# Optimization experiments

Hardware: AMD Instinct MI355X
Metric: run time of the kernel (lower is better)

## Reference

```python
import jax, jax.numpy as jnp
import numpy as np

B1, B2, CHUNK, HID, T = 64, 16, 128, 64, 131072
N_CHUNKS = 128


def setup_inputs() -> dict:
    key = jax.random.key(0)
    ks = jax.random.split(key, 12)
    # positive prices so log(p) is finite
    p = jax.random.uniform(ks[0], (T, 2), jnp.float32) * 2.0 + 0.5
    inds = jax.random.randint(ks[1], (B1,), 0, 100000, dtype=jnp.int32)
    open_slices = jax.random.randint(ks[2], (B1, B2, 1), 0, T, dtype=jnp.int32)
    ls_probs = jax.random.uniform(ks[3], (B1, B2, 1, 1), jnp.float32)
    open_probs = jax.random.uniform(ks[4], (B1, B2, 1, 1), jnp.float32)
    open_hx = jax.random.normal(ks[5], (B1, B2, 2, HID), jnp.float32) * 0.1
    s = 1.0 / np.sqrt(HID)
    # torch nn.LSTM params: gate order i,f,g,o
    W_ih = jax.random.uniform(ks[6], (4 * HID, 2), jnp.float32, -s, s)
    W_hh = jax.random.uniform(ks[7], (4 * HID, HID), jnp.float32, -s, s)
    b_ih = jax.random.uniform(ks[8], (4 * HID,), jnp.float32, -s, s)
    b_hh = jax.random.uniform(ks[9], (4 * HID,), jnp.float32, -s, s)
    W_out = jax.random.uniform(ks[10], (1, HID), jnp.float32, -s, s)
    b_out = jax.random.uniform(ks[11], (1,), jnp.float32, -s, s)
    return {"inds": inds, "p": p, "ls_probs": ls_probs, "open_probs": open_probs,
            "open_slices": open_slices, "open_hx": open_hx,
            "W_ih": W_ih, "W_hh": W_hh, "b_ih": b_ih, "b_hh": b_hh,
            "W_out": W_out, "b_out": b_out, "n_chunks": N_CHUNKS}


def reference(inds, p, ls_probs, open_probs, open_slices, open_hx,
              W_ih, W_hh, b_ih, b_hh, W_out, b_out, n_chunks):
    b1, b2 = open_hx.shape[:2]
    hid = open_hx.shape[-1]
    C = CHUNK
    h0 = open_hx[:, :, 0, :].reshape(b1 * b2, hid)
    c0 = open_hx[:, :, 1, :].reshape(b1 * b2, hid)
    open_logp = jnp.log(p[open_slices])  # (b1, b2, 1, 2)
    # sliding-window gather base: idx[i,j,t] = inds[i] + j + t (per-chunk offset added in scan)
    base = (inds[:, None, None]
            + jnp.arange(b2, dtype=inds.dtype)[None, :, None]
            + jnp.arange(C, dtype=inds.dtype)[None, None, :])  # (b1, b2, C)
    bias = b_ih + b_hh

    def lstm_chunk(x, h, c):  # x: (N, C, 2)
        xg = x @ W_ih.T + bias  # precompute input projection: (N, C, 4H)
        def step(carry, xg_t):
            h, c = carry
            g = xg_t + h @ W_hh.T
            i, f, gg, o = jnp.split(g, 4, axis=-1)
            c = jax.nn.sigmoid(f) * c + jax.nn.sigmoid(i) * jnp.tanh(gg)
            h = jax.nn.sigmoid(o) * jnp.tanh(c)
            return (h, c), h
        (h, c), hs = jax.lax.scan(step, (h, c), xg.swapaxes(0, 1))
        return hs.swapaxes(0, 1), h, c  # (N, C, H)

    def chunk_step(carry, offset):
        h, c, last_nd, loss = carry
        idx = base + offset * C                      # (b1, b2, C)
        p_chunk = p[idx]                             # (b1, b2, C, 2)
        x = p_chunk - p_chunk[:, :, :1, :]           # re-center on first step of chunk
        out, h, c = lstm_chunk(x.reshape(b1 * b2, C, 2), h, c)
        probs = jax.nn.sigmoid(out.reshape(b1, b2, C, hid) @ W_out.T + b_out)  # (b1,b2,C,1)
        not_done = last_nd * jnp.cumprod(1.0 - probs[:, :, :-1], axis=2)       # (b1,b2,C-1,1)
        probs = jnp.concatenate([probs[:, :, :1], probs[:, :, 1:] * not_done], axis=2)
        last_nd = not_done[:, :, -1:, :]
        logp = jnp.log(p_chunk)
        payoff = ls_probs * (logp - open_logp) + (1.0 - ls_probs) * (open_logp - logp)
        loss = loss + jnp.sum(open_probs * probs * payoff)
        return (h, c, last_nd, loss), None

    init = (h0, c0, jnp.ones((b1, b2, 1, 1), p.dtype), jnp.zeros((), p.dtype))
    (_, _, _, loss), _ = jax.lax.scan(chunk_step, init, jnp.arange(n_chunks))
    return loss
```

## Files before the change

kernel.cpp:

```cpp
#include <hip/hip_runtime.h>


#define CH  128
#define HID 64

__device__ __forceinline__ float rlf(float v, int l) {
  return __builtin_bit_cast(float, __builtin_amdgcn_readlane(__builtin_bit_cast(int, v), l));
}
__device__ __forceinline__ int rli(int v, int l) { return __builtin_amdgcn_readlane(v, l); }
__device__ __forceinline__ int packh(float a, float b) {
  return __builtin_bit_cast(int, __builtin_amdgcn_cvt_pkrtz(a, b));
}
__device__ __forceinline__ float frcp(float x) { return __builtin_amdgcn_rcpf(x); }
__device__ __forceinline__ float sigm(float x) { return frcp(1.0f + __expf(-x)); }
__device__ __forceinline__ float tanh_(float x) {
  float e = __expf(2.0f * x);
  return 1.0f - 2.0f * frcp(e + 1.0f);
}
template <int CTRL, int RMASK>
__device__ __forceinline__ float dpp_add(float v) {
  int x = __builtin_amdgcn_update_dpp(0, __builtin_bit_cast(int, v), CTRL, RMASK, 0xF, true);
  return v + __builtin_bit_cast(float, x);
}
__device__ __forceinline__ float dpp_xor1(float v) {
  int x = __builtin_amdgcn_update_dpp(0, __builtin_bit_cast(int, v), 0xB1, 0xF, 0xF, true);
  return __builtin_bit_cast(float, x);
}
__device__ __forceinline__ float dpp_wave_sum(float v) {
  v = dpp_add<0x111, 0xF>(v);
  v = dpp_add<0x112, 0xF>(v);
  v = dpp_add<0x114, 0xF>(v);
  v = dpp_add<0x118, 0xF>(v);
  v = dpp_add<0x142, 0xA>(v);
  v = dpp_add<0x143, 0xC>(v);
  return v;
}

#define DOTS(A, B, W) asm( \
  "v_dot2_f32_f16 %[a], %[h0], %[w0], %[a]\n\t"   \
  "v_dot2_f32_f16 %[b], %[h16], %[w16], %[b]\n\t" \
  "v_dot2_f32_f16 %[a], %[h1], %[w1], %[a]\n\t"   \
  "v_dot2_f32_f16 %[b], %[h17], %[w17], %[b]\n\t" \
  "v_dot2_f32_f16 %[a], %[h2], %[w2], %[a]\n\t"   \
  "v_dot2_f32_f16 %[b], %[h18], %[w18], %[b]\n\t" \
  "v_dot2_f32_f16 %[a], %[h3], %[w3], %[a]\n\t"   \
  "v_dot2_f32_f16 %[b], %[h19], %[w19], %[b]\n\t" \
  "v_dot2_f32_f16 %[a], %[h4], %[w4], %[a]\n\t"   \
  "v_dot2_f32_f16 %[b], %[h20], %[w20], %[b]\n\t" \
  "v_dot2_f32_f16 %[a], %[h5], %[w5], %[a]\n\t"   \
  "v_dot2_f32_f16 %[b], %[h21], %[w21], %[b]\n\t" \
  "v_dot2_f32_f16 %[a], %[h6], %[w6], %[a]\n\t"   \
  "v_dot2_f32_f16 %[b], %[h22], %[w22], %[b]\n\t" \
  "v_dot2_f32_f16 %[a], %[h7], %[w7], %[a]\n\t"   \
  "v_dot2_f32_f16 %[b], %[h23], %[w23], %[b]\n\t" \
  "v_dot2_f32_f16 %[a], %[h8], %[w8], %[a]\n\t"   \
  "v_dot2_f32_f16 %[b], %[h24], %[w24], %[b]\n\t" \
  "v_dot2_f32_f16 %[a], %[h9], %[w9], %[a]\n\t"   \
  "v_dot2_f32_f16 %[b], %[h25], %[w25], %[b]\n\t" \
  "v_dot2_f32_f16 %[a], %[h10], %[w10], %[a]\n\t" \
  "v_dot2_f32_f16 %[b], %[h26], %[w26], %[b]\n\t" \
  "v_dot2_f32_f16 %[a], %[h11], %[w11], %[a]\n\t" \
  "v_dot2_f32_f16 %[b], %[h27], %[w27], %[b]\n\t" \
  "v_dot2_f32_f16 %[a], %[h12], %[w12], %[a]\n\t" \
  "v_dot2_f32_f16 %[b], %[h28], %[w28], %[b]\n\t" \
  "v_dot2_f32_f16 %[a], %[h13], %[w13], %[a]\n\t" \
  "v_dot2_f32_f16 %[b], %[h29], %[w29], %[b]\n\t" \
  "v_dot2_f32_f16 %[a], %[h14], %[w14], %[a]\n\t" \
  "v_dot2_f32_f16 %[b], %[h30], %[w30], %[b]\n\t" \
  "v_dot2_f32_f16 %[a], %[h15], %[w15], %[a]\n\t" \
  "v_dot2_f32_f16 %[b], %[h31], %[w31], %[b]"     \
  : [a] "+v"(A), [b] "+v"(B) \
  : [h0] "s"(hs[0]),   [h1] "s"(hs[1]),   [h2] "s"(hs[2]),   [h3] "s"(hs[3]),   \
    [h4] "s"(hs[4]),   [h5] "s"(hs[5]),   [h6] "s"(hs[6]),   [h7] "s"(hs[7]),   \
    [h8] "s"(hs[8]),   [h9] "s"(hs[9]),   [h10] "s"(hs[10]), [h11] "s"(hs[11]), \
    [h12] "s"(hs[12]), [h13] "s"(hs[13]), [h14] "s"(hs[14]), [h15] "s"(hs[15]), \
    [h16] "s"(hs[16]), [h17] "s"(hs[17]), [h18] "s"(hs[18]), [h19] "s"(hs[19]), \
    [h20] "s"(hs[20]), [h21] "s"(hs[21]), [h22] "s"(hs[22]), [h23] "s"(hs[23]), \
    [h24] "s"(hs[24]), [h25] "s"(hs[25]), [h26] "s"(hs[26]), [h27] "s"(hs[27]), \
    [h28] "s"(hs[28]), [h29] "s"(hs[29]), [h30] "s"(hs[30]), [h31] "s"(hs[31]), \
    [w0] "v"(W[0]),   [w1] "v"(W[1]),   [w2] "v"(W[2]),   [w3] "v"(W[3]),   \
    [w4] "v"(W[4]),   [w5] "v"(W[5]),   [w6] "v"(W[6]),   [w7] "v"(W[7]),   \
    [w8] "v"(W[8]),   [w9] "v"(W[9]),   [w10] "v"(W[10]), [w11] "v"(W[11]), \
    [w12] "v"(W[12]), [w13] "v"(W[13]), [w14] "v"(W[14]), [w15] "v"(W[15]), \
    [w16] "v"(W[16]), [w17] "v"(W[17]), [w18] "v"(W[18]), [w19] "v"(W[19]), \
    [w20] "v"(W[20]), [w21] "v"(W[21]), [w22] "v"(W[22]), [w23] "v"(W[23]), \
    [w24] "v"(W[24]), [w25] "v"(W[25]), [w26] "v"(W[26]), [w27] "v"(W[27]), \
    [w28] "v"(W[28]), [w29] "v"(W[29]), [w30] "v"(W[30]), [w31] "v"(W[31]))

__global__ __attribute__((amdgpu_flat_work_group_size(128, 128), amdgpu_waves_per_eu(2, 2)))
void pc_lstm_kernel(const int* __restrict__ inds,
                    const float* __restrict__ p,
                    const float* __restrict__ ls_probs,
                    const float* __restrict__ open_probs,
                    const int* __restrict__ open_slices,
                    const float* __restrict__ open_hx,
                    const float* __restrict__ W_ih,
                    const float* __restrict__ W_hh,
                    const float* __restrict__ b_ih,
                    const float* __restrict__ b_hh,
                    const float* __restrict__ W_out,
                    const float* __restrict__ b_out,
                    const int* __restrict__ n_chunks_p,
                    float* __restrict__ out)
{
  __shared__ __fp16 ring[2][CH][HID];
  __shared__ int prod;
  __shared__ int cons;

  const int tid  = threadIdx.x;
  const int wv   = tid >> 6;
  const int lane = tid & 63;
  const int s    = blockIdx.x;
  const int n_chunks = n_chunks_p[0];
  const int tbase = inds[s >> 4] + (s & 15);
  const float2* p2 = (const float2*)p;

  if (tid == 0) { prod = 0; cons = 0; }
  __syncthreads();

  if (wv == 0) {
    int W0[32], W1[32], W2[32], W3[32];
    {
      const float2* r0 = (const float2*)(W_hh + (0 * HID + lane) * HID);
      const float2* r1 = (const float2*)(W_hh + (1 * HID + lane) * HID);
      const float2* r2 = (const float2*)(W_hh + (2 * HID + lane) * HID);
      const float2* r3 = (const float2*)(W_hh + (3 * HID + lane) * HID);
#pragma unroll
      for (int j = 0; j < 32; ++j) {
        float2 v0 = r0[j], v1 = r1[j], v2 = r2[j], v3 = r3[j];
        W0[j] = packh(v0.x, v0.y);
        W1[j] = packh(v1.x, v1.y);
        W2[j] = packh(v2.x, v2.y);
        W3[j] = packh(v3.x, v3.y);
      }
    }
    float wxa[4], wxb[4], bb[4];
#pragma unroll
    for (int g = 0; g < 4; ++g) {
      const int r = g * HID + lane;
      wxa[g] = W_ih[2 * r];
      wxb[g] = W_ih[2 * r + 1];
      bb[g]  = b_ih[r] + b_hh[r];
    }
    float h = open_hx[(s * 2 + 0) * HID + lane];
    float c = open_hx[(s * 2 + 1) * HID + lane];

    float2 curA = p2[tbase + lane];
    float2 curB = p2[tbase + HID + lane];
    float2 nxtA = curA, nxtB = curB;

    for (int off = 0; off < n_chunks; ++off) {
      if (off) { curA = nxtA; curB = nxtB; }
      const float px0 = rlf(curA.x, 0);
      const float px1 = rlf(curA.y, 0);
      float2 xA, xB;
      xA.x = curA.x - px0; xA.y = curA.y - px1;
      xB.x = curB.x - px0; xB.y = curB.y - px1;
      if (off + 1 < n_chunks) {
        const int nb = tbase + (off + 1) * CH;
        nxtA = p2[nb + lane];
        nxtB = p2[nb + HID + lane];
      }
      while (__hip_atomic_load(&cons, __ATOMIC_ACQUIRE, __HIP_MEMORY_SCOPE_WORKGROUP) + 2 <= off)
        __builtin_amdgcn_s_sleep(8);

      __fp16* slot = &ring[off & 1][0][0];
#pragma unroll
      for (int hf = 0; hf < 2; ++hf) {
        const float xcx = hf ? xB.x : xA.x;
        const float xcy = hf ? xB.y : xA.y;
#pragma unroll 1
        for (int tl = 0; tl < 64; ++tl) {
          const int hp = packh(h, dpp_xor1(h));
          int hs[32];
#pragma unroll
          for (int j = 0; j < 32; ++j) hs[j] = rli(hp, 2 * j);

          const float x0 = rlf(xcx, tl);
          const float x1 = rlf(xcy, tl);

          float A0 = fmaf(x0, wxa[0], bb[0]), B0 = x1 * wxb[0];
          float A1 = fmaf(x0, wxa[1], bb[1]), B1 = x1 * wxb[1];
          float A2 = fmaf(x0, wxa[2], bb[2]), B2 = x1 * wxb[2];
          float A3 = fmaf(x0, wxa[3], bb[3]), B3 = x1 * wxb[3];

          DOTS(A0, B0, W0);
          DOTS(A1, B1, W1);
          DOTS(A2, B2, W2);
          DOTS(A3, B3, W3);

          const float ig = sigm(A0 + B0);
          const float fg = sigm(A1 + B1);
          const float gg = tanh_(A2 + B2);
          const float og = sigm(A3 + B3);
          c = fmaf(fg, c, ig * gg);
          h = og * tanh_(c);

          slot[(hf * 64 + tl) * HID + lane] = (__fp16)h;
        }
      }
      if (lane == 0)
        __hip_atomic_store(&prod, off + 1, __ATOMIC_RELEASE, __HIP_MEMORY_SCOPE_WORKGROUP);
    }
  } else {
    const float wo   = W_out[lane];
    const float bout = b_out[0];
    const int   os   = open_slices[s];
    const float OL   = __logf(p[2 * os]) + __logf(p[2 * os + 1]);
    const float coef = open_probs[s] * (2.0f * ls_probs[s] - 1.0f);

    float S = 1.0f, D = 1.0f, lsum = 0.0f, psum = 0.0f;

    for (int off = 0; off < n_chunks; ++off) {
      const int cb = tbase + off * CH;
      const float2 cA = p2[cb + lane];
      const float2 cB = p2[cb + HID + lane];
      const float LA = __logf(cA.x) + __logf(cA.y);
      const float LB = __logf(cB.x) + __logf(cB.y);

      while (__hip_atomic_load(&prod, __ATOMIC_ACQUIRE, __HIP_MEMORY_SCOPE_WORKGROUP) <= off)
        __builtin_amdgcn_s_sleep(32);

      const __fp16* slot = &ring[off & 1][0][0];
#pragma unroll 1
      for (int tt = 0; tt < CH; ++tt) {
        const float hv = (float)slot[tt * HID + lane];
        const float z  = rlf(dpp_wave_sum(hv * wo), 63);
        const float pr = sigm(z + bout);
        const float Lt = (tt < 64) ? rlf(LA, tt) : rlf(LB, tt - 64);
        const float pn = (tt == 0) ? pr : pr * D;
        lsum = fmaf(pn, Lt, lsum);
        psum += pn;
        if (tt == 0)           D = S * (1.0f - pr);
        else if (tt < CH - 1)  D *= (1.0f - pr);
        else                   S = D;
      }
      if (lane == 0)
        __hip_atomic_store(&cons, off + 1, __ATOMIC_RELEASE, __HIP_MEMORY_SCOPE_WORKGROUP);
    }
    if (lane == 0) atomicAdd(out, coef * (lsum - OL * psum));
  }
}

extern "C" void kernel_launch(void* const* d_in, const int* in_sizes, int n_in,
                              void* d_out, int out_size, void* d_ws, size_t ws_size,
                              hipStream_t stream) {
  (void)hipMemsetAsync(d_out, 0, sizeof(float), stream);

  pc_lstm_kernel<<<dim3(1024), dim3(128), 0, stream>>>(
      (const int*)d_in[0],
      (const float*)d_in[1],
      (const float*)d_in[2],
      (const float*)d_in[3],
      (const int*)d_in[4],
      (const float*)d_in[5],
      (const float*)d_in[6],
      (const float*)d_in[7],
      (const float*)d_in[8],
      (const float*)d_in[9],
      (const float*)d_in[10],
      (const float*)d_in[11],
      (const int*)d_in[12],
      (float*)d_out);
}
```

Measured before the change: 7.947 ms.

## Replace scalar-broadcast dot2 recurrent matvec with MFMA reading h from LDS

Each recurrent step previously broadcast the packed fp16 h vector into scalar registers with readlanes and ran 128 v_dot2 instructions per lane against register-held W_hh rows. It now keeps W_hh in fp16 MFMA B-fragments in registers and reads the previous h row back from the LDS ring, which the step already writes. It then computes all 256 gate pre-activations with 32 16x16x32 f16 MFMAs and selects each lane's gate value from the accumulator layout. The goal is to move the matvec onto the matrix cores and drop the readlane broadcast. The cost is that most MFMA output rows are redundant and every step now waits on an LDS write-then-read round trip on the serial path.

```diff
diff --git a/kernel.cpp b/kernel.cpp
--- a/kernel.cpp
+++ b/kernel.cpp
@@ -4,12 +4,11 @@
 #define CH  128
 #define HID 64
 
+typedef __fp16 half8 __attribute__((ext_vector_type(8)));
+typedef float  f32x4 __attribute__((ext_vector_type(4)));
+
 __device__ __forceinline__ float rlf(float v, int l) {
   return __builtin_bit_cast(float, __builtin_amdgcn_readlane(__builtin_bit_cast(int, v), l));
-}
-__device__ __forceinline__ int rli(int v, int l) { return __builtin_amdgcn_readlane(v, l); }
-__device__ __forceinline__ int packh(float a, float b) {
-  return __builtin_bit_cast(int, __builtin_amdgcn_cvt_pkrtz(a, b));
 }
 __device__ __forceinline__ float frcp(float x) { return __builtin_amdgcn_rcpf(x); }
 __device__ __forceinline__ float sigm(float x) { return frcp(1.0f + __expf(-x)); }
@@ -21,10 +20,6 @@
 __device__ __forceinline__ float dpp_add(float v) {
   int x = __builtin_amdgcn_update_dpp(0, __builtin_bit_cast(int, v), CTRL, RMASK, 0xF, true);
   return v + __builtin_bit_cast(float, x);
-}
-__device__ __forceinline__ float dpp_xor1(float v) {
-  int x = __builtin_amdgcn_update_dpp(0, __builtin_bit_cast(int, v), 0xB1, 0xF, 0xF, true);
-  return __builtin_bit_cast(float, x);
 }
 __device__ __forceinline__ float dpp_wave_sum(float v) {
   v = dpp_add<0x111, 0xF>(v);
@@ -35,57 +30,6 @@
   v = dpp_add<0x143, 0xC>(v);
   return v;
 }
-
-#define DOTS(A, B, W) asm( \
-  "v_dot2_f32_f16 %[a], %[h0], %[w0], %[a]\n\t"   \
-  "v_dot2_f32_f16 %[b], %[h16], %[w16], %[b]\n\t" \
-  "v_dot2_f32_f16 %[a], %[h1], %[w1], %[a]\n\t"   \
-  "v_dot2_f32_f16 %[b], %[h17], %[w17], %[b]\n\t" \
-  "v_dot2_f32_f16 %[a], %[h2], %[w2], %[a]\n\t"   \
-  "v_dot2_f32_f16 %[b], %[h18], %[w18], %[b]\n\t" \
-  "v_dot2_f32_f16 %[a], %[h3], %[w3], %[a]\n\t"   \
-  "v_dot2_f32_f16 %[b], %[h19], %[w19], %[b]\n\t" \
-  "v_dot2_f32_f16 %[a], %[h4], %[w4], %[a]\n\t"   \
-  "v_dot2_f32_f16 %[b], %[h20], %[w20], %[b]\n\t" \
-  "v_dot2_f32_f16 %[a], %[h5], %[w5], %[a]\n\t"   \
-  "v_dot2_f32_f16 %[b], %[h21], %[w21], %[b]\n\t" \
-  "v_dot2_f32_f16 %[a], %[h6], %[w6], %[a]\n\t"   \
-  "v_dot2_f32_f16 %[b], %[h22], %[w22], %[b]\n\t" \
-  "v_dot2_f32_f16 %[a], %[h7], %[w7], %[a]\n\t"   \
-  "v_dot2_f32_f16 %[b], %[h23], %[w23], %[b]\n\t" \
-  "v_dot2_f32_f16 %[a], %[h8], %[w8], %[a]\n\t"   \
-  "v_dot2_f32_f16 %[b], %[h24], %[w24], %[b]\n\t" \
-  "v_dot2_f32_f16 %[a], %[h9], %[w9], %[a]\n\t"   \
-  "v_dot2_f32_f16 %[b], %[h25], %[w25], %[b]\n\t" \
-  "v_dot2_f32_f16 %[a], %[h10], %[w10], %[a]\n\t" \
-  "v_dot2_f32_f16 %[b], %[h26], %[w26], %[b]\n\t" \
-  "v_dot2_f32_f16 %[a], %[h11], %[w11], %[a]\n\t" \
-  "v_dot2_f32_f16 %[b], %[h27], %[w27], %[b]\n\t" \
-  "v_dot2_f32_f16 %[a], %[h12], %[w12], %[a]\n\t" \
-  "v_dot2_f32_f16 %[b], %[h28], %[w28], %[b]\n\t" \
-  "v_dot2_f32_f16 %[a], %[h13], %[w13], %[a]\n\t" \
-  "v_dot2_f32_f16 %[b], %[h29], %[w29], %[b]\n\t" \
-  "v_dot2_f32_f16 %[a], %[h14], %[w14], %[a]\n\t" \
-  "v_dot2_f32_f16 %[b], %[h30], %[w30], %[b]\n\t" \
-  "v_dot2_f32_f16 %[a], %[h15], %[w15], %[a]\n\t" \
-  "v_dot2_f32_f16 %[b], %[h31], %[w31], %[b]"     \
-  : [a] "+v"(A), [b] "+v"(B) \
-  : [h0] "s"(hs[0]),   [h1] "s"(hs[1]),   [h2] "s"(hs[2]),   [h3] "s"(hs[3]),   \
-    [h4] "s"(hs[4]),   [h5] "s"(hs[5]),   [h6] "s"(hs[6]),   [h7] "s"(hs[7]),   \
-    [h8] "s"(hs[8]),   [h9] "s"(hs[9]),   [h10] "s"(hs[10]), [h11] "s"(hs[11]), \
-    [h12] "s"(hs[12]), [h13] "s"(hs[13]), [h14] "s"(hs[14]), [h15] "s"(hs[15]), \
-    [h16] "s"(hs[16]), [h17] "s"(hs[17]), [h18] "s"(hs[18]), [h19] "s"(hs[19]), \
-    [h20] "s"(hs[20]), [h21] "s"(hs[21]), [h22] "s"(hs[22]), [h23] "s"(hs[23]), \
-    [h24] "s"(hs[24]), [h25] "s"(hs[25]), [h26] "s"(hs[26]), [h27] "s"(hs[27]), \
-    [h28] "s"(hs[28]), [h29] "s"(hs[29]), [h30] "s"(hs[30]), [h31] "s"(hs[31]), \
-    [w0] "v"(W[0]),   [w1] "v"(W[1]),   [w2] "v"(W[2]),   [w3] "v"(W[3]),   \
-    [w4] "v"(W[4]),   [w5] "v"(W[5]),   [w6] "v"(W[6]),   [w7] "v"(W[7]),   \
-    [w8] "v"(W[8]),   [w9] "v"(W[9]),   [w10] "v"(W[10]), [w11] "v"(W[11]), \
-    [w12] "v"(W[12]), [w13] "v"(W[13]), [w14] "v"(W[14]), [w15] "v"(W[15]), \
-    [w16] "v"(W[16]), [w17] "v"(W[17]), [w18] "v"(W[18]), [w19] "v"(W[19]), \
-    [w20] "v"(W[20]), [w21] "v"(W[21]), [w22] "v"(W[22]), [w23] "v"(W[23]), \
-    [w24] "v"(W[24]), [w25] "v"(W[25]), [w26] "v"(W[26]), [w27] "v"(W[27]), \
-    [w28] "v"(W[28]), [w29] "v"(W[29]), [w30] "v"(W[30]), [w31] "v"(W[31]))
 
 __global__ __attribute__((amdgpu_flat_work_group_size(128, 128), amdgpu_waves_per_eu(2, 2)))
 void pc_lstm_kernel(const int* __restrict__ inds,
@@ -119,21 +63,22 @@
   __syncthreads();
 
   if (wv == 0) {
-    int W0[32], W1[32], W2[32], W3[32];
-    {
-      const float2* r0 = (const float2*)(W_hh + (0 * HID + lane) * HID);
-      const float2* r1 = (const float2*)(W_hh + (1 * HID + lane) * HID);
-      const float2* r2 = (const float2*)(W_hh + (2 * HID + lane) * HID);
-      const float2* r3 = (const float2*)(W_hh + (3 * HID + lane) * HID);
-#pragma unroll
-      for (int j = 0; j < 32; ++j) {
-        float2 v0 = r0[j], v1 = r1[j], v2 = r2[j], v3 = r3[j];
-        W0[j] = packh(v0.x, v0.y);
-        W1[j] = packh(v1.x, v1.y);
-        W2[j] = packh(v2.x, v2.y);
-        W3[j] = packh(v3.x, v3.y);
-      }
-    }
+    const int kg = lane >> 4;
+    const int cc = lane & 15;
+
+    half8 Wb[32];
+#pragma unroll
+    for (int t = 0; t < 16; ++t) {
+#pragma unroll
+      for (int kc = 0; kc < 2; ++kc) {
+        const float* wp = W_hh + (16 * t + cc) * HID + 32 * kc + 8 * kg;
+        half8 w;
+#pragma unroll
+        for (int j = 0; j < 8; ++j) w[j] = (__fp16)wp[j];
+        Wb[2 * t + kc] = w;
+      }
+    }
+
     float wxa[4], wxb[4], bb[4];
 #pragma unroll
     for (int g = 0; g < 4; ++g) {
@@ -144,6 +89,13 @@
     }
     float h = open_hx[(s * 2 + 0) * HID + lane];
     float c = open_hx[(s * 2 + 1) * HID + lane];
+
+    ring[1][CH - 1][lane] = (__fp16)h;
+    const __fp16* arow = &ring[1][CH - 1][0];
+
+    const bool u1 = (lane & 16) != 0;
+    const bool u2 = (lane & 32) != 0;
+    const f32x4 zero4 = {0.f, 0.f, 0.f, 0.f};
 
     float2 curA = p2[tbase + lane];
     float2 curB = p2[tbase + HID + lane];
@@ -171,32 +123,40 @@
         const float xcy = hf ? xB.y : xA.y;
 #pragma unroll 1
         for (int tl = 0; tl < 64; ++tl) {
-          const int hp = packh(h, dpp_xor1(h));
-          int hs[32];
-#pragma unroll
-          for (int j = 0; j < 32; ++j) hs[j] = rli(hp, 2 * j);
+          const char* ab = (const char*)arow + 16 * kg;
+          const half8 a0 = *(const half8*)(ab);
+          const half8 a1 = *(const half8*)(ab + 64);
 
           const float x0 = rlf(xcx, tl);
           const float x1 = rlf(xcy, tl);
 
-          float A0 = fmaf(x0, wxa[0], bb[0]), B0 = x1 * wxb[0];
-          float A1 = fmaf(x0, wxa[1], bb[1]), B1 = x1 * wxb[1];
-          float A2 = fmaf(x0, wxa[2], bb[2]), B2 = x1 * wxb[2];
-          float A3 = fmaf(x0, wxa[3], bb[3]), B3 = x1 * wxb[3];
-
-          DOTS(A0, B0, W0);
-          DOTS(A1, B1, W1);
-          DOTS(A2, B2, W2);
-          DOTS(A3, B3, W3);
-
-          const float ig = sigm(A0 + B0);
-          const float fg = sigm(A1 + B1);
-          const float gg = tanh_(A2 + B2);
-          const float og = sigm(A3 + B3);
+          float pre[16];
+#pragma unroll
+          for (int t = 0; t < 16; ++t) {
+            f32x4 acc = __builtin_amdgcn_mfma_f32_16x16x32_f16(a0, Wb[2 * t],     zero4, 0, 0, 0);
+            acc       = __builtin_amdgcn_mfma_f32_16x16x32_f16(a1, Wb[2 * t + 1], acc,   0, 0, 0);
+            pre[t] = acc[0];
+          }
+
+          float pa[4];
+#pragma unroll
+          for (int g = 0; g < 4; ++g) {
+            const float s01 = u1 ? pre[4 * g + 1] : pre[4 * g + 0];
+            const float s23 = u1 ? pre[4 * g + 3] : pre[4 * g + 2];
+            const float dg  = u2 ? s23 : s01;
+            pa[g] = fmaf(x0, wxa[g], fmaf(x1, wxb[g], dg + bb[g]));
+          }
+
+          const float ig = sigm(pa[0]);
+          const float fg = sigm(pa[1]);
+          const float gg = tanh_(pa[2]);
+          const float og = sigm(pa[3]);
           c = fmaf(fg, c, ig * gg);
           h = og * tanh_(c);
 
-          slot[(hf * 64 + tl) * HID + lane] = (__fp16)h;
+          const int tt = hf * 64 + tl;
+          slot[tt * HID + lane] = (__fp16)h;
+          arow = &slot[tt * HID];
         }
       }
       if (lane == 0)
```

Result: slower. 11.30 ms (+42.1%).
